# Kernel optimization log

Measured on AMD Instinct MI355X. Metric: run time of the kernel, lower is better.

Reference implementation:

```python
import jax, jax.numpy as jnp
import numpy as np
from math import pi

N = 20000        # nodes
E = 640000       # edges (avg degree 32)
H = 128          # hidden_channels = num_filters
NB = 3           # num_bond_features
NGS = 50 - NB    # gaussians in smearing (num_gaussians - num_bond_features)
CUT = 10.0       # cutoff
L = 3            # num_interactions
B = 16           # graphs in batch
LOG2 = 0.6931471805599453


def ssp(x):
    # ShiftedSoftplus
    return jax.nn.softplus(x) - LOG2


def setup_inputs() -> dict:
    key = jax.random.key(0)
    ks = jax.random.split(key, 20)
    s = 0.05
    inp = {
        "z": jax.random.randint(ks[0], (N,), 0, 100),
        "pos": jax.random.uniform(ks[1], (N, 3), jnp.float32),
        "batch": jnp.sort(jax.random.randint(ks[2], (N,), 0, B)),
        "edge_index": jax.random.randint(ks[3], (2, E), 0, N),
        "edge_attr": jax.random.uniform(ks[4], (E, NB), jnp.float32),
        # parameters (stacked over L interaction blocks where per-layer)
        "emb": jax.random.normal(ks[5], (100, H), jnp.float32) * s,
        "mlp_w1": jax.random.normal(ks[6], (L, NB + NGS, H), jnp.float32) * s,
        "mlp_b1": jnp.zeros((L, H), jnp.float32),
        "mlp_w2": jax.random.normal(ks[7], (L, H, H), jnp.float32) * s,
        "mlp_b2": jnp.zeros((L, H), jnp.float32),
        "cf1_w": jax.random.normal(ks[8], (L, H, H), jnp.float32) * s,   # lin1, no bias
        "cf2_w": jax.random.normal(ks[9], (L, H, H), jnp.float32) * s,
        "cf2_b": jnp.zeros((L, H), jnp.float32),
        "lin_w": jax.random.normal(ks[10], (L, H, H), jnp.float32) * s,
        "lin_b": jnp.zeros((L, H), jnp.float32),
        "out1_w": jax.random.normal(ks[11], (H, H // 2), jnp.float32) * s,
        "out1_b": jnp.zeros((H // 2,), jnp.float32),
        "out2_w": jax.random.normal(ks[12], (H // 2, 1), jnp.float32) * s,
        "out2_b": jnp.zeros((1,), jnp.float32),
    }
    return inp


def reference(z, pos, batch, edge_index, edge_attr, emb,
              mlp_w1, mlp_b1, mlp_w2, mlp_b2,
              cf1_w, cf2_w, cf2_b, lin_w, lin_b,
              out1_w, out1_b, out2_w, out2_b):
    row, col = edge_index[0], edge_index[1]  # source j, target i
    h = emb[z]                               # [N,H] embedding_e(z)
    # edge_weight = ||pos[row] - pos[col]||
    ew = jnp.linalg.norm(pos[row] - pos[col], axis=-1)  # [E]
    # GaussianSmearing(0, cutoff, NGS)
    offset = jnp.linspace(0.0, CUT, NGS, dtype=jnp.float32)
    coeff = -0.5 / (offset[1] - offset[0]) ** 2
    gs = jnp.exp(coeff * (ew[:, None] - offset[None, :]) ** 2)  # [E,NGS]
    ea = jnp.concatenate([edge_attr, gs], axis=1)  # [E,50]
    # cosine cutoff weight
    C = 0.5 * (jnp.cos(ew * pi / CUT) + 1.0)       # [E]
    for l in range(L):
        # filter MLP on edge features
        W = ssp(ea @ mlp_w1[l] + mlp_b1[l]) @ mlp_w2[l] + mlp_b2[l]  # [E,H]
        W = W * C[:, None]
        xh = h @ cf1_w[l]                    # lin1 (no bias) [N,H]
        msg = xh[row] * W                    # gather-mul [E,H]
        agg = jax.ops.segment_sum(msg, col, num_segments=N)  # scatter-add [N,H]
        xc = agg @ cf2_w[l] + cf2_b[l]       # lin2
        xc = ssp(xc)
        xc = xc @ lin_w[l] + lin_b[l]        # block output lin
        h = h + xc                           # residual
    h = ssp(h @ out1_w + out1_b)             # [N,H/2]
    per_node = h @ out2_w + out2_b           # [N,1]
    out = jax.ops.segment_sum(per_node, batch, num_segments=B)  # readout 'add' -> [B,1]
    return out
```

## Files before the change

### kernel.cpp

```cpp
#include <hip/hip_runtime.h>
#include <hip/hip_bf16.h>

typedef __attribute__((ext_vector_type(8))) short bfrag;
typedef __attribute__((ext_vector_type(4))) float f32x4;

__device__ __forceinline__ float ssp_f(float x) {
    return fmaxf(x, 0.f) + __logf(1.f + __expf(-fabsf(x))) - 0.6931471805599453f;
}

__device__ __forceinline__ unsigned short f2b(float x) {
    __hip_bfloat16 h = __float2bfloat16(x);
    return *(unsigned short*)&h;
}

__device__ __forceinline__ unsigned int pk2(float a, float b) {
    __hip_bfloat162 h2 = __float22bfloat162_rn(make_float2(a, b));
    return *(unsigned int*)&h2;
}

__global__ void sniff_kernel(const unsigned int* __restrict__ raw, int* __restrict__ flag)
{
    __shared__ int cnt[256];
    const int t = threadIdx.x;
    unsigned int w = raw[t];
    unsigned int e = (w >> 7) & 0xFFu;
    cnt[t] = (e >= 100u && e <= 135u) ? 1 : 0;
    __syncthreads();
    for (int s = 128; s > 0; s >>= 1) {
        if (t < s) cnt[t] += cnt[t + s];
        __syncthreads();
    }
    if (t == 0) *flag = (cnt[0] >= 160) ? 1 : 0;
}

__global__ void sniff_int_kernel(const unsigned int* __restrict__ z, int* __restrict__ iflag)
{
    __shared__ int cnt[128];
    const int t = threadIdx.x;
    cnt[t] = (z[2 * t + 1] == 0u) ? 1 : 0;
    __syncthreads();
    for (int s = 64; s > 0; s >>= 1) {
        if (t < s) cnt[t] += cnt[t + s];
        __syncthreads();
    }
    if (t == 0) *iflag = (cnt[0] >= 126) ? 1 : 0;
}

struct Cvt16 {
    const void* src[16];
    long off[17];
};

__global__ __launch_bounds__(256) void convert_fused_kernel(
    Cvt16 args, float* __restrict__ F, long total, const int* __restrict__ flag)
{
    long i = (long)blockIdx.x * 256 + threadIdx.x;
    if (i >= total) return;
    int lo = 0, hi = 16;
    while (hi - lo > 1) {
        int mid = (lo + hi) >> 1;
        if (i >= args.off[mid]) lo = mid; else hi = mid;
    }
    long loc = i - args.off[lo];
    if (*flag) F[i] = __bfloat162float(((const __hip_bfloat16*)args.src[lo])[loc]);
    else       F[i] = ((const float*)args.src[lo])[loc];
}

__global__ __launch_bounds__(256) void convert_int_kernel(
    const void* __restrict__ src, int* __restrict__ dst, int n,
    const int* __restrict__ iflag)
{
    int i = blockIdx.x * 256 + threadIdx.x;
    if (i >= n) return;
    if (*iflag) dst[i] = (int)(((const long long*)src)[i]);
    else        dst[i] = ((const int*)src)[i];
}

__global__ __launch_bounds__(256) void embed_kernel(
    const int* __restrict__ z, const float* __restrict__ embf,
    float* __restrict__ h, int NH)
{
    int idx = blockIdx.x * 256 + threadIdx.x;
    if (idx >= NH) return;
    h[idx] = embf[z[idx >> 7] * 128 + (idx & 127)];
}

__global__ __launch_bounds__(256) void zero_int_kernel(int* p, int n)
{
    int i = blockIdx.x * 256 + threadIdx.x;
    if (i < n) p[i] = 0;
}

__global__ __launch_bounds__(256) void hist_kernel(const int* __restrict__ col,
                                                   int* __restrict__ count, int E)
{
    int e = blockIdx.x * 256 + threadIdx.x;
    if (e < E) atomicAdd(&count[col[e]], 1);
}

__global__ __launch_bounds__(256) void scan_kernel(const int* __restrict__ count,
                                                   int* __restrict__ rowptr,
                                                   int* __restrict__ next, int N)
{
    __shared__ int part[256];
    const int t = threadIdx.x;
    const int chunk = (N + 255) / 256;
    const int lo = t * chunk, hi = min(lo + chunk, N);
    int s = 0;
    for (int i = lo; i < hi; ++i) s += count[i];
    part[t] = s;
    __syncthreads();
    if (t == 0) {
        int run = 0;
        for (int i = 0; i < 256; ++i) { int v = part[i]; part[i] = run; run += v; }
        rowptr[N] = run;
    }
    __syncthreads();
    int run = part[t];
    for (int i = lo; i < hi; ++i) {
        rowptr[i] = run; next[i] = run;
        run += count[i];
    }
}

__global__ __launch_bounds__(256) void prep_scatter_kernel(
    const float* __restrict__ posf, const int* __restrict__ row,
    const int* __restrict__ col, const float* __restrict__ eattrf,
    int* __restrict__ next,
    int* __restrict__ rowS, int* __restrict__ colS,
    float* __restrict__ CS, float* __restrict__ ewS,
    unsigned short* __restrict__ eaS, int E, int NB)
{
    int e = blockIdx.x * 256 + threadIdx.x;
    if (e >= E) return;
    const int r = row[e], c = col[e];
    const int p = atomicAdd(&next[c], 1);
    float dx = posf[r*3+0] - posf[c*3+0];
    float dy = posf[r*3+1] - posf[c*3+1];
    float dz = posf[r*3+2] - posf[c*3+2];
    float ew = sqrtf(dx*dx + dy*dy + dz*dz);
    rowS[p] = r; colS[p] = c; ewS[p] = ew;
    CS[p] = 0.5f * (cosf(ew * 0.3141592653589793f) + 1.0f);
    unsigned short* o = eaS + (long)p * 4;
    for (int q = 0; q < 4; ++q)
        o[q] = (q < NB) ? f2b(eattrf[(long)e * NB + q]) : (unsigned short)0;
}

__global__ __launch_bounds__(256) void wtrans_kernel(
    const float* __restrict__ src, unsigned short* __restrict__ dst,
    int K, int Kpad, int N)
{
    int idx = blockIdx.x * 256 + threadIdx.x;
    if (idx >= N * Kpad) return;
    int n = idx / Kpad, k = idx - n * Kpad;
    dst[idx] = (k < K) ? f2b(src[k * N + n]) : (unsigned short)0;
}

__global__ __launch_bounds__(256) void wtrans_node_kernel(
    const float* __restrict__ cf1, const float* __restrict__ cf2,
    const float* __restrict__ lin, unsigned short* __restrict__ dst, int total)
{
    int idx = blockIdx.x * 256 + threadIdx.x;
    if (idx >= total) return;
    int m = idx >> 14;
    int fam = m % 3, l = m / 3;
    int local = idx & 16383;
    int n = local >> 7, k = local & 127;
    const float* src = (fam == 0 ? cf1 : fam == 1 ? cf2 : lin) + (long)l * 16384;
    dst[idx] = f2b(src[k * 128 + n]);
}

template<int MODE>
__global__ __launch_bounds__(256) void node_gemm_tiled(
    const float* __restrict__ in, const float* __restrict__ W,
    const float* __restrict__ bias, float* __restrict__ out, int N)
{
    __shared__ float in_s[32][128];
    const int t = threadIdx.x;
    const long n0 = (long)blockIdx.x * 32;
    for (int i = t; i < 32 * 128; i += 256) {
        long n = n0 + (i >> 7);
        in_s[i >> 7][i & 127] = (n < N) ? in[n * 128 + (i & 127)] : 0.f;
    }
    __syncthreads();
    const int j = t & 31, sub = t >> 5;
    const int c4 = j * 4, rb = sub * 4;
    float acc[4][4];
    float4 bv = make_float4(0.f, 0.f, 0.f, 0.f);
    if (MODE != 0) bv = *(const float4*)(bias + c4);
    #pragma unroll
    for (int i = 0; i < 4; ++i) { acc[i][0]=bv.x; acc[i][1]=bv.y; acc[i][2]=bv.z; acc[i][3]=bv.w; }
    #pragma unroll 4
    for (int k = 0; k < 128; ++k) {
        const float4 wv = *(const float4*)(W + k * 128 + c4);
        #pragma unroll
        for (int i = 0; i < 4; ++i) {
            const float a = in_s[rb + i][k];
            acc[i][0] += a * wv.x; acc[i][1] += a * wv.y;
            acc[i][2] += a * wv.z; acc[i][3] += a * wv.w;
        }
    }
    #pragma unroll
    for (int i = 0; i < 4; ++i) {
        long n = n0 + rb + i;
        if (n >= N) continue;
        float4 o;
        if (MODE == 1) {
            o.x = ssp_f(acc[i][0]); o.y = ssp_f(acc[i][1]);
            o.z = ssp_f(acc[i][2]); o.w = ssp_f(acc[i][3]);
        } else {
            o.x = acc[i][0]; o.y = acc[i][1]; o.z = acc[i][2]; o.w = acc[i][3];
        }
        if (MODE == 2) {
            float4 p = *(const float4*)(out + n * 128 + c4);
            o.x += p.x; o.y += p.y; o.z += p.z; o.w += p.w;
        }
        *(float4*)(out + n * 128 + c4) = o;
    }
}

__global__ __launch_bounds__(256) void node_gemm1_embed_mfma(
    const int* __restrict__ zi, const float* __restrict__ embf,
    const unsigned short* __restrict__ wt,
    float* __restrict__ h, float* __restrict__ out, float* __restrict__ aggz, int N)
{
    __shared__ __align__(16) short a_b[16][136];
    const int t = threadIdx.x;
    const long r0 = (long)blockIdx.x * 16;
    const float4 z4 = make_float4(0.f, 0.f, 0.f, 0.f);
    #pragma unroll
    for (int j = 0; j < 2; ++j) {
        const int fi = t + j * 256;
        const int r = fi >> 5, c4 = (fi & 31) << 2;
        const long n = r0 + r;
        float4 v = z4;
        if (n < N) {
            v = *(const float4*)(embf + (long)zi[n] * 128 + c4);
            *(float4*)(h + n * 128 + c4) = v;
            *(float4*)(aggz + n * 128 + c4) = z4;
        }
        *(uint2*)&a_b[r][c4] = make_uint2(pk2(v.x, v.y), pk2(v.z, v.w));
    }
    __syncthreads();
    const int lane = t & 63, w = t >> 6;
    const int colL = lane & 15, quad = lane >> 4;
    const int nh = w * 32;
    f32x4 acc[2];
    #pragma unroll
    for (int tt = 0; tt < 2; ++tt) acc[tt] = (f32x4){0.f, 0.f, 0.f, 0.f};
    #pragma unroll
    for (int ks = 0; ks < 4; ++ks) {
        const bfrag a = *(const bfrag*)&a_b[colL][ks * 32 + quad * 8];
        #pragma unroll
        for (int tt = 0; tt < 2; ++tt) {
            const bfrag wf = *(const bfrag*)&wt[(long)(nh + tt * 16 + colL) * 128 + ks * 32 + quad * 8];
            acc[tt] = __builtin_amdgcn_mfma_f32_16x16x32_bf16(wf, a, acc[tt], 0, 0, 0);
        }
    }
    const long node = r0 + colL;
    if (node < N) {
        float* orow = out + node * 128;
        #pragma unroll
        for (int tt = 0; tt < 2; ++tt) {
            const int c0 = nh + tt * 16 + quad * 4;
            *(float4*)(orow + c0) = make_float4(acc[tt][0], acc[tt][1], acc[tt][2], acc[tt][3]);
        }
    }
}

template<int CHAIN>
__global__ __launch_bounds__(256) void node_gemm23_mfma(
    const float* __restrict__ in,
    const unsigned short* __restrict__ w1t, const float* __restrict__ b1,
    const unsigned short* __restrict__ w2t, const float* __restrict__ b2,
    float* __restrict__ h,
    const unsigned short* __restrict__ cf1t, float* __restrict__ xh,
    float* __restrict__ aggz, int N)
{
    __shared__ __align__(16) short a_b[16][136];
    __shared__ __align__(16) short t_b[16][136];
    const int t = threadIdx.x;
    const long r0 = (long)blockIdx.x * 16;
    #pragma unroll
    for (int j = 0; j < 2; ++j) {
        const int fi = t + j * 256;
        const int r = fi >> 5, c4 = (fi & 31) << 2;
        const long n = r0 + r;
        float4 v = make_float4(0.f, 0.f, 0.f, 0.f);
        if (n < N) v = *(const float4*)(in + n * 128 + c4);
        *(uint2*)&a_b[r][c4] = make_uint2(pk2(v.x, v.y), pk2(v.z, v.w));
    }
    __syncthreads();
    const int lane = t & 63, w = t >> 6;
    const int colL = lane & 15, quad = lane >> 4;
    const int nh = w * 32;
    {
        f32x4 acc[2];
        #pragma unroll
        for (int tt = 0; tt < 2; ++tt) acc[tt] = (f32x4){0.f, 0.f, 0.f, 0.f};
        #pragma unroll
        for (int ks = 0; ks < 4; ++ks) {
            const bfrag a = *(const bfrag*)&a_b[colL][ks * 32 + quad * 8];
            #pragma unroll
            for (int tt = 0; tt < 2; ++tt) {
                const bfrag wf = *(const bfrag*)&w1t[(long)(nh + tt * 16 + colL) * 128 + ks * 32 + quad * 8];
                acc[tt] = __builtin_amdgcn_mfma_f32_16x16x32_bf16(wf, a, acc[tt], 0, 0, 0);
            }
        }
        #pragma unroll
        for (int tt = 0; tt < 2; ++tt) {
            const int c0 = nh + tt * 16 + quad * 4;
            const float4 bv = *(const float4*)(b1 + c0);
            const float v0 = ssp_f(acc[tt][0] + bv.x);
            const float v1 = ssp_f(acc[tt][1] + bv.y);
            const float v2 = ssp_f(acc[tt][2] + bv.z);
            const float v3 = ssp_f(acc[tt][3] + bv.w);
            *(uint2*)&t_b[colL][c0] = make_uint2(pk2(v0, v1), pk2(v2, v3));
        }
    }
    __syncthreads();
    {
        f32x4 acc[2];
        #pragma unroll
        for (int tt = 0; tt < 2; ++tt) acc[tt] = (f32x4){0.f, 0.f, 0.f, 0.f};
        #pragma unroll
        for (int ks = 0; ks < 4; ++ks) {
            const bfrag a = *(const bfrag*)&t_b[colL][ks * 32 + quad * 8];
            #pragma unroll
            for (int tt = 0; tt < 2; ++tt) {
                const bfrag wf = *(const bfrag*)&w2t[(long)(nh + tt * 16 + colL) * 128 + ks * 32 + quad * 8];
                acc[tt] = __builtin_amdgcn_mfma_f32_16x16x32_bf16(wf, a, acc[tt], 0, 0, 0);
            }
        }
        const long node = r0 + colL;
        if (node < N) {
            float* hrow = h + node * 128;
            #pragma unroll
            for (int tt = 0; tt < 2; ++tt) {
                const int c0 = nh + tt * 16 + quad * 4;
                const float4 bv = *(const float4*)(b2 + c0);
                float4 hv = *(const float4*)(hrow + c0);
                hv.x += acc[tt][0] + bv.x;
                hv.y += acc[tt][1] + bv.y;
                hv.z += acc[tt][2] + bv.z;
                hv.w += acc[tt][3] + bv.w;
                *(float4*)(hrow + c0) = hv;
                if (CHAIN)
                    *(uint2*)&a_b[colL][c0] = make_uint2(pk2(hv.x, hv.y), pk2(hv.z, hv.w));
            }
        }
    }
    if (CHAIN) {
        __syncthreads();
        f32x4 acc[2];
        #pragma unroll
        for (int tt = 0; tt < 2; ++tt) acc[tt] = (f32x4){0.f, 0.f, 0.f, 0.f};
        #pragma unroll
        for (int ks = 0; ks < 4; ++ks) {
            const bfrag a = *(const bfrag*)&a_b[colL][ks * 32 + quad * 8];
            #pragma unroll
            for (int tt = 0; tt < 2; ++tt) {
                const bfrag wf = *(const bfrag*)&cf1t[(long)(nh + tt * 16 + colL) * 128 + ks * 32 + quad * 8];
                acc[tt] = __builtin_amdgcn_mfma_f32_16x16x32_bf16(wf, a, acc[tt], 0, 0, 0);
            }
        }
        const long node = r0 + colL;
        if (node < N) {
            float* orow = xh + node * 128;
            float* zrow = aggz + node * 128;
            const float4 z = make_float4(0.f, 0.f, 0.f, 0.f);
            #pragma unroll
            for (int tt = 0; tt < 2; ++tt) {
                const int c0 = nh + tt * 16 + quad * 4;
                *(float4*)(orow + c0) = make_float4(acc[tt][0], acc[tt][1], acc[tt][2], acc[tt][3]);
                *(float4*)(zrow + c0) = z;
            }
        }
    }
}

__global__ __launch_bounds__(256, 8) void edge_mfma(
    const int* __restrict__ rowS, const int* __restrict__ colS,
    const float* __restrict__ CS, const float* __restrict__ ewS,
    const unsigned short* __restrict__ eaS,
    const unsigned short* __restrict__ w1t, const float* __restrict__ b1,
    const unsigned short* __restrict__ w2t, const float* __restrict__ b2,
    const float* __restrict__ xh, float* __restrict__ agg,
    int E, int NB, int F50, float delta, float coeff)
{
    __shared__ __align__(16) char smem[32 * 132 * 4];
    short (*ea_b)[64]    = (short(*)[64])smem;
    short (*t_b)[128]    = (short(*)[128])(smem + 4096);
    float (*runbuf)[132] = (float(*)[132])smem;
    __shared__ int   col_s[32];
    __shared__ float ew_s[32];

    const int t = threadIdx.x;
    const long p0 = (long)blockIdx.x * 32;
    const int lane = t & 63;
    const int w    = t >> 6;
    const int colL = lane & 15;
    const int quad = lane >> 4;
    const int m0   = (w & 1) * 16;
    const int ebase = m0 + quad * 4;

    int   row_r[4];
    float C_r[4];
    if (p0 + 32 <= E) {
        const int4   rv = *(const int4*)&rowS[p0 + ebase];
        const float4 cv = *(const float4*)&CS[p0 + ebase];
        row_r[0] = rv.x; row_r[1] = rv.y; row_r[2] = rv.z; row_r[3] = rv.w;
        C_r[0] = cv.x; C_r[1] = cv.y; C_r[2] = cv.z; C_r[3] = cv.w;
    } else {
        #pragma unroll
        for (int reg = 0; reg < 4; ++reg) {
            long p = p0 + ebase + reg;
            const long pc = (p < E) ? p : E - 1;
            row_r[reg] = rowS[pc];
            C_r[reg]   = (p < E) ? CS[pc] : 0.f;
        }
    }
    float xv[4][4];
    #pragma unroll
    for (int reg = 0; reg < 4; ++reg) {
        const float* xr = xh + (long)row_r[reg] * 128;
        #pragma unroll
        for (int tt = 0; tt < 4; ++tt)
            xv[reg][tt] = xr[((w >> 1) * 4 + tt) * 16 + colL];
    }

    {
        const int t32 = t & 31;
        long p = p0 + t32; if (p >= E) p = E - 1;
        col_s[t32] = colS[p];
        ew_s[t32]  = ewS[p];
    }
    for (int i = t; i < 32 * 64; i += 256) {
        const int e = i >> 6, k = i & 63;
        long p = p0 + e; if (p >= E) p = E - 1;
        unsigned short v;
        if (k < NB)        v = eaS[p * 4 + k];
        else if (k < F50) {
            float d = ew_s[e] - (float)(k - NB) * delta;
            v = f2b(__expf(coeff * d * d));
        } else             v = 0;
        ea_b[e][k ^ ((e & 7) << 3)] = (short)v;
    }
    __syncthreads();

    {
        f32x4 acc[4];
        #pragma unroll
        for (int tt = 0; tt < 4; ++tt) acc[tt] = (f32x4){0.f, 0.f, 0.f, 0.f};
        const int ar  = m0 + colL;
        const int asw = (ar & 7) << 3;
        #pragma unroll
        for (int ks = 0; ks < 2; ++ks) {
            const bfrag a = *(const bfrag*)&ea_b[ar][(ks * 32 + quad * 8) ^ asw];
            #pragma unroll
            for (int tt = 0; tt < 4; ++tt) {
                const int n0 = ((w >> 1) * 4 + tt) * 16;
                const bfrag b = *(const bfrag*)&w1t[(long)(n0 + colL) * 64 + ks * 32 + quad * 8];
                acc[tt] = __builtin_amdgcn_mfma_f32_16x16x32_bf16(a, b, acc[tt], 0, 0, 0);
            }
        }
        #pragma unroll
        for (int tt = 0; tt < 4; ++tt) {
            const int n0 = ((w >> 1) * 4 + tt) * 16;
            const float bcol = b1[n0 + colL];
            #pragma unroll
            for (int reg = 0; reg < 4; ++reg) {
                const int rr = m0 + quad * 4 + reg;
                float v = ssp_f(acc[tt][reg] + bcol);
                t_b[rr][(n0 + colL) ^ ((rr & 7) << 3)] = (short)f2b(v);
            }
        }
    }
    __syncthreads();

    {
        f32x4 acc[4];
        #pragma unroll
        for (int tt = 0; tt < 4; ++tt) acc[tt] = (f32x4){0.f, 0.f, 0.f, 0.f};
        const int ar  = m0 + colL;
        const int asw = (ar & 7) << 3;
        #pragma unroll
        for (int ks = 0; ks < 4; ++ks) {
            const bfrag a = *(const bfrag*)&t_b[ar][(ks * 32 + quad * 8) ^ asw];
            #pragma unroll
            for (int tt = 0; tt < 4; ++tt) {
                const int n0 = ((w >> 1) * 4 + tt) * 16;
                const bfrag b = *(const bfrag*)&w2t[(long)(n0 + colL) * 128 + ks * 32 + quad * 8];
                acc[tt] = __builtin_amdgcn_mfma_f32_16x16x32_bf16(a, b, acc[tt], 0, 0, 0);
            }
        }
        __syncthreads();
        #pragma unroll
        for (int tt = 0; tt < 4; ++tt) {
            const int n0 = ((w >> 1) * 4 + tt) * 16;
            const int cg = n0 + colL;
            const float bcol = b2[cg];
            #pragma unroll
            for (int reg = 0; reg < 4; ++reg) {
                const int e = ebase + reg;
                const float v = acc[tt][reg] + bcol;
                runbuf[e][cg] = v * C_r[reg] * xv[reg][tt];
            }
        }
    }
    __syncthreads();

    {
        const int cc   = t & 127;
        const int e0h  = (t >> 7) * 16;
        float a     = runbuf[e0h][cc];
        int  curcol = col_s[e0h];
        #pragma unroll 4
        for (int e = e0h + 1; e < e0h + 16; ++e) {
            const int c2 = col_s[e];
            if (c2 != curcol) {
                atomicAdd(&agg[(long)curcol * 128 + cc], a);
                a = 0.f; curcol = c2;
            }
            a += runbuf[e][cc];
        }
        atomicAdd(&agg[(long)curcol * 128 + cc], a);
    }
}

__global__ __launch_bounds__(256) void edge_atomic(
    const float* __restrict__ posf,
    const int* __restrict__ row, const int* __restrict__ col,
    const float* __restrict__ eattrf,
    const float* __restrict__ w1, const float* __restrict__ b1,
    const float* __restrict__ w2, const float* __restrict__ b2,
    const float* __restrict__ xh, float* __restrict__ agg,
    int E, int NB, int F50, float delta, float coeff)
{
    __shared__ float ea_s[32][52];
    __shared__ float t_s[32][128];
    __shared__ int   row_s[32];
    __shared__ int   col_s[32];
    __shared__ float C_s[32];
    __shared__ float ew_s[32];

    const int t = threadIdx.x;
    const long e0 = (long)blockIdx.x * 32;

    if (t < 32) {
        long e = e0 + t; if (e >= E) e = E - 1;
        const int r = row[e], c = col[e];
        row_s[t] = r; col_s[t] = c;
        float dx = posf[r*3+0] - posf[c*3+0];
        float dy = posf[r*3+1] - posf[c*3+1];
        float dz = posf[r*3+2] - posf[c*3+2];
        float ew = sqrtf(dx*dx + dy*dy + dz*dz);
        ew_s[t] = ew;
        C_s[t]  = (e0 + t < E) ? 0.5f * (cosf(ew * 0.3141592653589793f) + 1.0f) : 0.f;
        for (int q = 0; q < NB; ++q)
            ea_s[t][q] = eattrf[e * NB + q];
    }
    __syncthreads();
    {
        const int NGS = F50 - NB;
        for (int i = t; i < 32 * NGS; i += 256) {
            const int e = i / NGS, g = i - e * NGS;
            const float d = ew_s[e] - (float)g * delta;
            ea_s[e][NB + g] = __expf(coeff * d * d);
        }
    }
    __syncthreads();

    const int j = t & 31, sub = t >> 5;
    const int c4 = j * 4, eb = sub * 4;
    float acc[4][4];
    {
        const float4 bv = *(const float4*)(b1 + c4);
        #pragma unroll
        for (int i = 0; i < 4; ++i) { acc[i][0]=bv.x; acc[i][1]=bv.y; acc[i][2]=bv.z; acc[i][3]=bv.w; }
        for (int k = 0; k < F50; ++k) {
            const float4 wv = *(const float4*)(w1 + k * 128 + c4);
            #pragma unroll
            for (int i = 0; i < 4; ++i) {
                const float a = ea_s[eb + i][k];
                acc[i][0] += a * wv.x; acc[i][1] += a * wv.y;
                acc[i][2] += a * wv.z; acc[i][3] += a * wv.w;
            }
        }
        #pragma unroll
        for (int i = 0; i < 4; ++i) {
            float4 o;
            o.x = ssp_f(acc[i][0]); o.y = ssp_f(acc[i][1]);
            o.z = ssp_f(acc[i][2]); o.w = ssp_f(acc[i][3]);
            *(float4*)&t_s[eb + i][c4] = o;
        }
    }
    __syncthreads();
    {
        const float4 bv = *(const float4*)(b2 + c4);
        #pragma unroll
        for (int i = 0; i < 4; ++i) { acc[i][0]=bv.x; acc[i][1]=bv.y; acc[i][2]=bv.z; acc[i][3]=bv.w; }
        #pragma unroll 4
        for (int k = 0; k < 128; ++k) {
            const float4 wv = *(const float4*)(w2 + k * 128 + c4);
            #pragma unroll
            for (int i = 0; i < 4; ++i) {
                const float a = t_s[eb + i][k];
                acc[i][0] += a * wv.x; acc[i][1] += a * wv.y;
                acc[i][2] += a * wv.z; acc[i][3] += a * wv.w;
            }
        }
    }
    #pragma unroll
    for (int i = 0; i < 4; ++i) {
        const int e = eb + i;
        if (e0 + e >= E) continue;
        const float Ce = C_s[e];
        const float4 xv = *(const float4*)(xh + (long)row_s[e] * 128 + c4);
        float* ag = agg + (long)col_s[e] * 128 + c4;
        atomicAdd(ag + 0, acc[i][0] * Ce * xv.x);
        atomicAdd(ag + 1, acc[i][1] * Ce * xv.y);
        atomicAdd(ag + 2, acc[i][2] * Ce * xv.z);
        atomicAdd(ag + 3, acc[i][3] * Ce * xv.w);
    }
}

__global__ __launch_bounds__(256) void readout_mfma(
    const float* __restrict__ h, const unsigned short* __restrict__ o1t,
    const float* __restrict__ o1b, const float* __restrict__ o2w,
    const float* __restrict__ o2b, const int* __restrict__ batch,
    float* __restrict__ accb, int N)
{
    __shared__ __align__(16) short a_b[16][136];
    __shared__ float nb[16];
    const int t = threadIdx.x;
    const long r0 = (long)blockIdx.x * 16;
    #pragma unroll
    for (int j = 0; j < 2; ++j) {
        const int fi = t + j * 256;
        const int r = fi >> 5, c4 = (fi & 31) << 2;
        const long n = r0 + r;
        float4 v = make_float4(0.f, 0.f, 0.f, 0.f);
        if (n < N) v = *(const float4*)(h + n * 128 + c4);
        *(uint2*)&a_b[r][c4] = make_uint2(pk2(v.x, v.y), pk2(v.z, v.w));
    }
    if (t < 16) nb[t] = 0.f;
    __syncthreads();
    const int lane = t & 63, w = t >> 6;
    const int colL = lane & 15, quad = lane >> 4;
    const int nh = w * 16;
    f32x4 acc = (f32x4){0.f, 0.f, 0.f, 0.f};
    #pragma unroll
    for (int ks = 0; ks < 4; ++ks) {
        const bfrag a = *(const bfrag*)&a_b[colL][ks * 32 + quad * 8];
        const bfrag wf = *(const bfrag*)&o1t[(long)(nh + colL) * 128 + ks * 32 + quad * 8];
        acc = __builtin_amdgcn_mfma_f32_16x16x32_bf16(wf, a, acc, 0, 0, 0);
    }
    float s = 0.f;
    {
        const int c0 = nh + quad * 4;
        const float4 bv = *(const float4*)(o1b + c0);
        const float4 wv = *(const float4*)(o2w + c0);
        s += ssp_f(acc[0] + bv.x) * wv.x;
        s += ssp_f(acc[1] + bv.y) * wv.y;
        s += ssp_f(acc[2] + bv.z) * wv.z;
        s += ssp_f(acc[3] + bv.w) * wv.w;
    }
    s += __shfl_xor(s, 16);
    s += __shfl_xor(s, 32);
    if (quad == 0) atomicAdd(&nb[colL], s);
    __syncthreads();
    if (t < 16) {
        const long node = r0 + t;
        if (node < N) atomicAdd(&accb[batch[node]], nb[t] + o2b[0]);
    }
}

__global__ __launch_bounds__(128) void readout_simple(
    const float* __restrict__ h,
    const float* __restrict__ o1w, const float* __restrict__ o1b,
    const float* __restrict__ o2w, const float* __restrict__ o2b,
    const int* __restrict__ batch, float* __restrict__ accb)
{
    __shared__ float hr[128];
    __shared__ float vv[64];
    const int n = blockIdx.x;
    const int t = threadIdx.x;
    hr[t] = h[(long)n * 128 + t];
    __syncthreads();
    if (t < 64) {
        float a = o1b[t];
        #pragma unroll 8
        for (int k = 0; k < 128; ++k)
            a = fmaf(hr[k], o1w[k * 64 + t], a);
        vv[t] = ssp_f(a) * o2w[t];
    }
    __syncthreads();
    if (t < 32) vv[t] += vv[t + 32];
    __syncthreads();
    if (t < 16) vv[t] += vv[t + 16];
    __syncthreads();
    if (t < 8)  vv[t] += vv[t + 8];
    __syncthreads();
    if (t < 4)  vv[t] += vv[t + 4];
    __syncthreads();
    if (t < 2)  vv[t] += vv[t + 2];
    __syncthreads();
    if (t == 0) atomicAdd(&accb[batch[n]], vv[0] + vv[1] + o2b[0]);
}

__global__ void finalize_kernel(const float* __restrict__ accb,
                                float* __restrict__ out, int B)
{
    int t = blockIdx.x * 256 + threadIdx.x;
    if (t < B) out[t] = accb[t];
}

extern "C" void kernel_launch(void* const* d_in, const int* in_sizes, int n_in,
                              void* d_out, int out_size, void* d_ws, size_t ws_size,
                              hipStream_t stream)
{
    const int N   = in_sizes[0];
    const int E   = in_sizes[3] / 2;
    const int B   = out_size;
    const int H   = 128;
    const int L   = in_sizes[7] / H;
    const int NB  = in_sizes[4] / E;
    const int F50 = in_sizes[6] / (L * H);
    const int NGS = F50 - NB;
    const float delta = 10.0f / (float)(NGS - 1);
    const float coeff = -0.5f / (delta * delta);

    const int fidx[16] = {1, 4, 5, 6, 7, 8, 9, 10, 11, 12, 13, 14, 15, 16, 17, 18};
    Cvt16 cv;
    cv.off[0] = 0;
    for (int i = 0; i < 16; ++i) {
        cv.src[i] = d_in[fidx[i]];
        cv.off[i + 1] = cv.off[i] + in_sizes[fidx[i]];
    }
    const long ftot = cv.off[16];

    float* F = (float*)d_ws;
    long base = (ftot + 3) & ~3L;
    float* h    = F + base;
    float* xh   = h + (long)N * H;
    float* agg  = xh + (long)N * H;
    float* accb = agg + (long)N * H;
    int*   flag  = (int*)(accb + ((B + 3) & ~3));
    int*   iflag = flag + 1;
    int*   zi     = flag + 4;
    int*   batchi = zi + N;
    int*   eidxi  = batchi + N;
    int*   count  = eidxi + 2 * E;
    int*   rowptr = count + N;
    int*   next   = rowptr + N + 1;
    int*   rowS   = next + N;
    int*   colS   = rowS + E;
    float* CS     = (float*)(colS + E);
    float* ewS    = CS + E;
    unsigned short* eaS = (unsigned short*)(ewS + E);
    unsigned short* w1t = eaS + 4L * E;
    unsigned short* w2t = w1t + (long)L * 128 * 64;
    unsigned short* nwt = w2t + (long)L * 128 * 128;
    unsigned short* o1t = nwt + 3L * L * 128 * 128;
    long used_bytes = (long)((char*)(o1t + 64 * 128) - (char*)d_ws);
    const bool use_fast = (used_bytes <= (long)ws_size) && (F50 <= 64) && (NB <= 4);

    sniff_kernel<<<1, 256, 0, stream>>>((const unsigned int*)d_in[5], flag);
    sniff_int_kernel<<<1, 128, 0, stream>>>((const unsigned int*)d_in[0], iflag);

    convert_fused_kernel<<<(int)((ftot + 255) / 256), 256, 0, stream>>>(cv, F, ftot, flag);
    convert_int_kernel<<<(N + 255) / 256, 256, 0, stream>>>(d_in[0], zi, N, iflag);
    convert_int_kernel<<<(N + 255) / 256, 256, 0, stream>>>(d_in[2], batchi, N, iflag);
    convert_int_kernel<<<(2 * E + 255) / 256, 256, 0, stream>>>(d_in[3], eidxi, 2 * E, iflag);

    const float* posf   = F + cv.off[0];
    const float* eattrf = F + cv.off[1];
    const float* embf   = F + cv.off[2];
    const float* w1   = F + cv.off[3];  const float* b1   = F + cv.off[4];
    const float* w2   = F + cv.off[5];  const float* b2   = F + cv.off[6];
    const float* cf1  = F + cv.off[7];  const float* cf2  = F + cv.off[8];
    const float* cf2b = F + cv.off[9];  const float* lin  = F + cv.off[10];
    const float* linb = F + cv.off[11]; const float* o1   = F + cv.off[12];
    const float* o1b  = F + cv.off[13]; const float* o2   = F + cv.off[14];
    const float* o2b  = F + cv.off[15];

    if (use_fast) {
        zero_int_kernel<<<(N + 255) / 256, 256, 0, stream>>>(count, N);
        hist_kernel<<<(E + 255) / 256, 256, 0, stream>>>(eidxi + E, count, E);
        scan_kernel<<<1, 256, 0, stream>>>(count, rowptr, next, N);
        prep_scatter_kernel<<<(E + 255) / 256, 256, 0, stream>>>(
            posf, eidxi, eidxi + E, eattrf, next, rowS, colS, CS, ewS, eaS, E, NB);
        for (int l = 0; l < L; ++l) {
            wtrans_kernel<<<(128 * 64 + 255) / 256, 256, 0, stream>>>(
                w1 + (long)l * F50 * H, w1t + (long)l * 128 * 64, F50, 64, 128);
            wtrans_kernel<<<(128 * 128 + 255) / 256, 256, 0, stream>>>(
                w2 + (long)l * H * H, w2t + (long)l * 128 * 128, 128, 128, 128);
        }
        const int ntot = 3 * L * 128 * 128;
        wtrans_node_kernel<<<(ntot + 255) / 256, 256, 0, stream>>>(cf1, cf2, lin, nwt, ntot);
        wtrans_kernel<<<(64 * 128 + 255) / 256, 256, 0, stream>>>(o1, o1t, 128, 128, 64);
    }

    hipMemsetAsync(accb, 0, (size_t)B * sizeof(float), stream);

    const int ngemm16 = (N + 15) / 16;
    const int nedge   = (E + 31) / 32;
    if (use_fast) {
        node_gemm1_embed_mfma<<<ngemm16, 256, 0, stream>>>(
            zi, embf, nwt + 0, h, xh, agg, N);
        for (int l = 0; l < L; ++l) {
            edge_mfma<<<nedge, 256, 0, stream>>>(
                rowS, colS, CS, ewS, eaS,
                w1t + (long)l * 128 * 64, b1 + (long)l * H,
                w2t + (long)l * 128 * 128, b2 + (long)l * H,
                xh, agg, E, NB, F50, delta, coeff);
            if (l < L - 1) {
                node_gemm23_mfma<1><<<ngemm16, 256, 0, stream>>>(
                    agg, nwt + (long)(l * 3 + 1) * 16384, cf2b + (long)l * H,
                    nwt + (long)(l * 3 + 2) * 16384, linb + (long)l * H, h,
                    nwt + (long)((l + 1) * 3 + 0) * 16384, xh, agg, N);
            } else {
                node_gemm23_mfma<0><<<ngemm16, 256, 0, stream>>>(
                    agg, nwt + (long)(l * 3 + 1) * 16384, cf2b + (long)l * H,
                    nwt + (long)(l * 3 + 2) * 16384, linb + (long)l * H, h,
                    nullptr, nullptr, nullptr, N);
            }
        }
        readout_mfma<<<ngemm16, 256, 0, stream>>>(h, o1t, o1b, o2, o2b, batchi, accb, N);
    } else {
        embed_kernel<<<(N * H + 255) / 256, 256, 0, stream>>>(zi, embf, h, N * H);
        const int ngemm32 = (N + 31) / 32;
        for (int l = 0; l < L; ++l) {
            hipMemsetAsync(agg, 0, (size_t)N * H * sizeof(float), stream);
            node_gemm_tiled<0><<<ngemm32, 256, 0, stream>>>(h, cf1 + (long)l * H * H, nullptr, xh, N);
            edge_atomic<<<nedge, 256, 0, stream>>>(
                posf, eidxi, eidxi + E, eattrf,
                w1 + (long)l * F50 * H, b1 + (long)l * H,
                w2 + (long)l * H * H,  b2 + (long)l * H,
                xh, agg, E, NB, F50, delta, coeff);
            node_gemm_tiled<1><<<ngemm32, 256, 0, stream>>>(agg, cf2 + (long)l * H * H, cf2b + (long)l * H, xh, N);
            node_gemm_tiled<2><<<ngemm32, 256, 0, stream>>>(xh, lin + (long)l * H * H, linb + (long)l * H, h, N);
        }
        readout_simple<<<N, 128, 0, stream>>>(h, o1, o1b, o2, o2b, batchi, accb);
    }
    finalize_kernel<<<(B + 255) / 256, 256, 0, stream>>>(accb, (float*)d_out, B);
}
```

Baseline: 1.454 ms.

## Fuse weight transposes and scatter edge messages directly from MFMA registers

Merges the eight separate weight-transpose launches into one kernel. In the edge kernel, the shared-memory staging buffer and the extra barriers before the segmented scatter-add are removed. Each lane now run-length combines its four sorted edges in registers and issues atomics directly, and the xh gather is moved after the first MFMA to overlap with it. This cuts launches, LDS traffic and syncs, but issues more atomics, since runs are only merged over 4 edges instead of 16.

```diff
diff --git a/kernel.cpp b/kernel.cpp
--- a/kernel.cpp
+++ b/kernel.cpp
@@ -146,28 +146,41 @@
         o[q] = (q < NB) ? f2b(eattrf[(long)e * NB + q]) : (unsigned short)0;
 }
 
-__global__ __launch_bounds__(256) void wtrans_kernel(
-    const float* __restrict__ src, unsigned short* __restrict__ dst,
-    int K, int Kpad, int N)
-{
-    int idx = blockIdx.x * 256 + threadIdx.x;
-    if (idx >= N * Kpad) return;
-    int n = idx / Kpad, k = idx - n * Kpad;
-    dst[idx] = (k < K) ? f2b(src[k * N + n]) : (unsigned short)0;
-}
-
-__global__ __launch_bounds__(256) void wtrans_node_kernel(
+__global__ __launch_bounds__(256) void wtrans_all_kernel(
+    const float* __restrict__ w1, const float* __restrict__ w2,
     const float* __restrict__ cf1, const float* __restrict__ cf2,
-    const float* __restrict__ lin, unsigned short* __restrict__ dst, int total)
+    const float* __restrict__ lin, const float* __restrict__ o1,
+    unsigned short* __restrict__ w1t, unsigned short* __restrict__ w2t,
+    unsigned short* __restrict__ nwt, unsigned short* __restrict__ o1t,
+    int L, int F50, int total)
 {
     int idx = blockIdx.x * 256 + threadIdx.x;
     if (idx >= total) return;
-    int m = idx >> 14;
-    int fam = m % 3, l = m / 3;
-    int local = idx & 16383;
-    int n = local >> 7, k = local & 127;
-    const float* src = (fam == 0 ? cf1 : fam == 1 ? cf2 : lin) + (long)l * 16384;
-    dst[idx] = f2b(src[k * 128 + n]);
+    const int A  = L * 8192;
+    const int Bq = L * 16384;
+    const int Cq = 3 * L * 16384;
+    if (idx < A) {
+        const int l = idx >> 13, local = idx & 8191;
+        const int n = local >> 6, k = local & 63;
+        w1t[idx] = (k < F50) ? f2b(w1[(long)l * F50 * 128 + k * 128 + n]) : (unsigned short)0;
+    } else if (idx < A + Bq) {
+        const int j = idx - A;
+        const int l = j >> 14, local = j & 16383;
+        const int n = local >> 7, k = local & 127;
+        w2t[j] = f2b(w2[(long)l * 16384 + k * 128 + n]);
+    } else if (idx < A + Bq + Cq) {
+        const int j = idx - A - Bq;
+        const int m = j >> 14;
+        const int fam = m % 3, l = m / 3;
+        const int local = j & 16383;
+        const int n = local >> 7, k = local & 127;
+        const float* src = (fam == 0 ? cf1 : fam == 1 ? cf2 : lin) + (long)l * 16384;
+        nwt[j] = f2b(src[k * 128 + n]);
+    } else {
+        const int j = idx - A - Bq - Cq;
+        const int n = j >> 7, k = j & 127;
+        o1t[j] = f2b(o1[k * 64 + n]);
+    }
 }
 
 template<int MODE>
@@ -388,11 +401,8 @@
     const float* __restrict__ xh, float* __restrict__ agg,
     int E, int NB, int F50, float delta, float coeff)
 {
-    __shared__ __align__(16) char smem[32 * 132 * 4];
-    short (*ea_b)[64]    = (short(*)[64])smem;
-    short (*t_b)[128]    = (short(*)[128])(smem + 4096);
-    float (*runbuf)[132] = (float(*)[132])smem;
-    __shared__ int   col_s[32];
+    __shared__ __align__(16) short ea_b[32][64];
+    __shared__ __align__(16) short t_b[32][128];
     __shared__ float ew_s[32];
 
     const int t = threadIdx.x;
@@ -404,36 +414,30 @@
     const int m0   = (w & 1) * 16;
     const int ebase = m0 + quad * 4;
 
-    int   row_r[4];
+    int   row_r[4], col_r[4];
     float C_r[4];
     if (p0 + 32 <= E) {
         const int4   rv = *(const int4*)&rowS[p0 + ebase];
-        const float4 cv = *(const float4*)&CS[p0 + ebase];
+        const int4   cv = *(const int4*)&colS[p0 + ebase];
+        const float4 Cv = *(const float4*)&CS[p0 + ebase];
         row_r[0] = rv.x; row_r[1] = rv.y; row_r[2] = rv.z; row_r[3] = rv.w;
-        C_r[0] = cv.x; C_r[1] = cv.y; C_r[2] = cv.z; C_r[3] = cv.w;
+        col_r[0] = cv.x; col_r[1] = cv.y; col_r[2] = cv.z; col_r[3] = cv.w;
+        C_r[0] = Cv.x; C_r[1] = Cv.y; C_r[2] = Cv.z; C_r[3] = Cv.w;
     } else {
         #pragma unroll
         for (int reg = 0; reg < 4; ++reg) {
             long p = p0 + ebase + reg;
             const long pc = (p < E) ? p : E - 1;
             row_r[reg] = rowS[pc];
+            col_r[reg] = colS[pc];
             C_r[reg]   = (p < E) ? CS[pc] : 0.f;
         }
-    }
-    float xv[4][4];
-    #pragma unroll
-    for (int reg = 0; reg < 4; ++reg) {
-        const float* xr = xh + (long)row_r[reg] * 128;
-        #pragma unroll
-        for (int tt = 0; tt < 4; ++tt)
-            xv[reg][tt] = xr[((w >> 1) * 4 + tt) * 16 + colL];
     }
 
     {
         const int t32 = t & 31;
         long p = p0 + t32; if (p >= E) p = E - 1;
-        col_s[t32] = colS[p];
-        ew_s[t32]  = ewS[p];
+        ew_s[t32] = ewS[p];
     }
     for (int i = t; i < 32 * 64; i += 256) {
         const int e = i >> 6, k = i & 63;
@@ -448,6 +452,8 @@
     }
     __syncthreads();
 
+    float xv[4][4];
+
     {
         f32x4 acc[4];
         #pragma unroll
@@ -465,6 +471,13 @@
             }
         }
         #pragma unroll
+        for (int reg = 0; reg < 4; ++reg) {
+            const float* xr = xh + (long)row_r[reg] * 128;
+            #pragma unroll
+            for (int tt = 0; tt < 4; ++tt)
+                xv[reg][tt] = xr[((w >> 1) * 4 + tt) * 16 + colL];
+        }
+        #pragma unroll
         for (int tt = 0; tt < 4; ++tt) {
             const int n0 = ((w >> 1) * 4 + tt) * 16;
             const float bcol = b1[n0 + colL];
@@ -494,37 +507,23 @@
                 acc[tt] = __builtin_amdgcn_mfma_f32_16x16x32_bf16(a, b, acc[tt], 0, 0, 0);
             }
         }
-        __syncthreads();
         #pragma unroll
         for (int tt = 0; tt < 4; ++tt) {
-            const int n0 = ((w >> 1) * 4 + tt) * 16;
-            const int cg = n0 + colL;
+            const int cg = ((w >> 1) * 4 + tt) * 16 + colL;
             const float bcol = b2[cg];
-            #pragma unroll
-            for (int reg = 0; reg < 4; ++reg) {
-                const int e = ebase + reg;
-                const float v = acc[tt][reg] + bcol;
-                runbuf[e][cg] = v * C_r[reg] * xv[reg][tt];
-            }
-        }
-    }
-    __syncthreads();
-
-    {
-        const int cc   = t & 127;
-        const int e0h  = (t >> 7) * 16;
-        float a     = runbuf[e0h][cc];
-        int  curcol = col_s[e0h];
-        #pragma unroll 4
-        for (int e = e0h + 1; e < e0h + 16; ++e) {
-            const int c2 = col_s[e];
-            if (c2 != curcol) {
-                atomicAdd(&agg[(long)curcol * 128 + cc], a);
-                a = 0.f; curcol = c2;
-            }
-            a += runbuf[e][cc];
-        }
-        atomicAdd(&agg[(long)curcol * 128 + cc], a);
+            float run = (acc[tt][0] + bcol) * C_r[0] * xv[0][tt];
+            int   cur = col_r[0];
+            #pragma unroll
+            for (int reg = 1; reg < 4; ++reg) {
+                const float msg = (acc[tt][reg] + bcol) * C_r[reg] * xv[reg][tt];
+                if (col_r[reg] != cur) {
+                    atomicAdd(&agg[(long)cur * 128 + cg], run);
+                    run = 0.f; cur = col_r[reg];
+                }
+                run += msg;
+            }
+            atomicAdd(&agg[(long)cur * 128 + cg], run);
+        }
     }
 }
 
@@ -791,15 +790,9 @@
         scan_kernel<<<1, 256, 0, stream>>>(count, rowptr, next, N);
         prep_scatter_kernel<<<(E + 255) / 256, 256, 0, stream>>>(
             posf, eidxi, eidxi + E, eattrf, next, rowS, colS, CS, ewS, eaS, E, NB);
-        for (int l = 0; l < L; ++l) {
-            wtrans_kernel<<<(128 * 64 + 255) / 256, 256, 0, stream>>>(
-                w1 + (long)l * F50 * H, w1t + (long)l * 128 * 64, F50, 64, 128);
-            wtrans_kernel<<<(128 * 128 + 255) / 256, 256, 0, stream>>>(
-                w2 + (long)l * H * H, w2t + (long)l * 128 * 128, 128, 128, 128);
-        }
-        const int ntot = 3 * L * 128 * 128;
-        wtrans_node_kernel<<<(ntot + 255) / 256, 256, 0, stream>>>(cf1, cf2, lin, nwt, ntot);
-        wtrans_kernel<<<(64 * 128 + 255) / 256, 256, 0, stream>>>(o1, o1t, 128, 128, 64);
+        const int wt_total = L * 8192 + L * 16384 + 3 * L * 16384 + 8192;
+        wtrans_all_kernel<<<(wt_total + 255) / 256, 256, 0, stream>>>(
+            w1, w2, cf1, cf2, lin, o1, w1t, w2t, nwt, o1t, L, F50, wt_total);
     }
 
     hipMemsetAsync(accb, 0, (size_t)B * sizeof(float), stream);
```

New measurement: 1.580 ms. 8.7% more time.
